# Optimization experiments

Hardware: AMD Instinct MI355X
Metric: run time of the kernel (lower is better)

## Reference

```python
import jax, jax.numpy as jnp
import numpy as np

WS = (7, 7, 7)
NUM_HEADS = 3
DIM = 96
GT_NUM = 1
NW = 64  # number of distinct window masks


def _relative_position_index(ws):
    # Faithful replication of the source's index construction (including its
    # idiosyncratic scale factors 3*ws[1]-1 and 2*ws[1]-1).
    cs = np.arange(ws[0]); ch = np.arange(ws[1]); cw = np.arange(ws[2])
    coords = np.stack(np.meshgrid(cs, ch, cw, indexing='ij'))  # [3, S, H, W]
    cf = coords.reshape(3, -1)                                  # [3, N_]
    rel = cf[:, :, None] - cf[:, None, :]                       # [3, N_, N_]
    rel = rel.transpose(1, 2, 0).copy()
    rel[:, :, 0] += ws[0] - 1
    rel[:, :, 1] += ws[1] - 1
    rel[:, :, 2] += ws[2] - 1
    rel[:, :, 0] *= 3 * ws[1] - 1
    rel[:, :, 1] *= 2 * ws[1] - 1
    return rel.sum(-1).astype(np.int32)                         # [N_, N_]


def setup_inputs() -> dict:
    key = jax.random.key(0)
    ks = jax.random.split(key, 8)
    N_ = WS[0] * WS[1] * WS[2]  # 343
    B_ = 512
    table_size = (2 * WS[0] - 1) * (2 * WS[1] - 1) * (2 * WS[2] - 1)  # 2197
    return {
        'x': jax.random.normal(ks[0], (B_, N_, DIM), jnp.float32),
        'gt': jax.random.normal(ks[1], (B_, GT_NUM, DIM), jnp.float32),
        'mask': jax.random.normal(ks[2], (NW, N_, N_), jnp.float32),
        'rel_index': jnp.asarray(_relative_position_index(WS)),
        'Wqkv': jax.random.normal(ks[3], (3 * DIM, DIM), jnp.float32) * 0.02,
        'b_qkv': jax.random.normal(ks[4], (3 * DIM,), jnp.float32) * 0.02,
        'Wproj': jax.random.normal(ks[5], (DIM, DIM), jnp.float32) * 0.02,
        'b_proj': jax.random.normal(ks[6], (DIM,), jnp.float32) * 0.02,
        'bias_table': jax.random.normal(ks[7], (table_size, NUM_HEADS), jnp.float32) * 0.02,
    }


def reference(x, gt, mask, rel_index, Wqkv, b_qkv, Wproj, b_proj, bias_table):
    B_, N_, C = x.shape
    g = gt.shape[1]
    H = NUM_HEADS
    hd = C // H
    scale = hd ** (-0.5)

    xc = jnp.concatenate([gt, x], axis=1)               # [B_, N, C]
    N = N_ + g
    qkv = xc @ Wqkv.T + b_qkv                           # [B_, N, 3C]
    qkv = qkv.reshape(B_, N, 3, H, hd).transpose(2, 0, 3, 1, 4)
    q, k, v = qkv[0], qkv[1], qkv[2]                    # [B_, H, N, hd]

    attn = jnp.einsum('bhnd,bhmd->bhnm', q * scale, k)  # [B_, H, N, N]

    # gathered relative-position bias: [N_, N_, H] -> [H, N_, N_]
    bias = bias_table[rel_index.reshape(-1)].reshape(N_, N_, H).transpose(2, 0, 1)

    nW = mask.shape[0]
    sub = attn[:, :, g:, g:] + bias[None]               # [B_, H, N_, N_]
    sub = sub.reshape(B_ // nW, nW, H, N_, N_) + mask[None, :, None]
    attn = attn.at[:, :, g:, g:].set(sub.reshape(B_, H, N_, N_))

    attn = jax.nn.softmax(attn, axis=-1)
    out = jnp.einsum('bhnm,bhmd->bhnd', attn, v)        # [B_, H, N, hd]
    out = out.transpose(0, 2, 1, 3).reshape(B_, N, C)
    out = out @ Wproj.T + b_proj

    gt_out = out[:, :-N_, :]
    x_out = out[:, -N_:, :]
    return (x_out, gt_out)
```

## Files before the change

### kernel.cpp

```cpp
#include <hip/hip_runtime.h>

typedef __attribute__((ext_vector_type(8))) _Float16 f16x8;
typedef __fp16 hpk2 __attribute__((ext_vector_type(2)));
typedef __attribute__((ext_vector_type(4))) float f32x4;

#define NB 512
#define NH 3
#define NSEQ 344
#define NPAD 352
#define NX 343
#define HD 32
#define CDIM 96
#define SP 352
#define SP2 (SP * SP)
#define SCALE 0.17677669529663687f

static __device__ __forceinline__ unsigned short f2h(float f) {
    _Float16 h = (_Float16)f;
    return __builtin_bit_cast(unsigned short, h);
}
static __device__ __forceinline__ f16x8 ld8(const unsigned short* p) {
    uint4 u = *(const uint4*)p;
    return __builtin_bit_cast(f16x8, u);
}

__global__ __launch_bounds__(256) void k_bias(
    const int* __restrict__ rel, const float* __restrict__ table,
    const float* __restrict__ mask, float* __restrict__ mp, float* __restrict__ bp)
{
    int idx = blockIdx.x * 256 + threadIdx.x;
    if (idx >= 67 * SP2) return;
    int s = idx / SP2; int rem2 = idx - s * SP2;
    int i = rem2 / SP, jj = rem2 - i * SP;
    bool valid = (i >= 1 && i < NSEQ && jj >= 1 && jj < NSEQ);
    if (s < 64) {
        float v = valid ? mask[(size_t)s * NX * NX + (i - 1) * NX + (jj - 1)] : 0.f;
        mp[(size_t)s * SP2 + rem2] = v;
    } else {
        int h = s - 64;
        float v = 0.f;
        if (valid) { int r = rel[(i - 1) * NX + (jj - 1)]; v = table[r * 3 + h]; }
        bp[(size_t)h * SP2 + rem2] = v;
    }
}

__global__ __launch_bounds__(256) void k_qkv(
    const float* __restrict__ x, const float* __restrict__ gt,
    const float* __restrict__ Wqkv, const float* __restrict__ bqkv,
    unsigned short* __restrict__ qs, unsigned short* __restrict__ ks,
    unsigned short* __restrict__ vs)
{
    __shared__ unsigned short Wb[288 * 104];
    int tid = threadIdx.x;
    for (int i = tid; i < 288 * 96; i += 256) {
        int c = i / 96, k = i - c * 96;
        Wb[c * 104 + k] = f2h(Wqkv[i]);
    }
    __syncthreads();
    int w = tid >> 6, l = tid & 63, la = l & 15, lg = l >> 4;

    int rowA = blockIdx.x * 64 + w * 16 + la;
    int bA = rowA / NSEQ, nA = rowA - bA * NSEQ;
    const float* srcA = (nA == 0) ? (gt + bA * CDIM) : (x + (bA * NX + (nA - 1)) * CDIM);
    f16x8 af[3];
#pragma unroll
    for (int kk = 0; kk < 3; ++kk) {
        float4 f0 = *(const float4*)&srcA[kk * 32 + lg * 8];
        float4 f1 = *(const float4*)&srcA[kk * 32 + lg * 8 + 4];
        f16x8 a;
        a[0] = (_Float16)f0.x; a[1] = (_Float16)f0.y; a[2] = (_Float16)f0.z; a[3] = (_Float16)f0.w;
        a[4] = (_Float16)f1.x; a[5] = (_Float16)f1.y; a[6] = (_Float16)f1.z; a[7] = (_Float16)f1.w;
        af[kk] = a;
    }
    f32x4 acc[18];
#pragma unroll
    for (int t = 0; t < 18; ++t) { acc[t][0]=0.f; acc[t][1]=0.f; acc[t][2]=0.f; acc[t][3]=0.f; }
#pragma unroll
    for (int t = 0; t < 18; ++t) {
#pragma unroll
        for (int kk = 0; kk < 3; ++kk) {
            f16x8 bf = ld8(&Wb[(t * 16 + la) * 104 + kk * 32 + lg * 8]);
            acc[t] = __builtin_amdgcn_mfma_f32_16x16x32_f16(af[kk], bf, acc[t], 0, 0, 0);
        }
    }
    int rowBase = blockIdx.x * 64 + w * 16 + lg * 4;
#pragma unroll
    for (int t = 0; t < 18; ++t) {
        int c = t * 16 + la;
        int s = c / 96;
        int rem = c - s * 96;
        int h = rem >> 5, d = rem & 31;
        float bq = bqkv[c];
        unsigned short* dst = (s == 0) ? qs : ((s == 1) ? ks : vs);
        float mul = (s == 0) ? SCALE : 1.0f;
#pragma unroll
        for (int r = 0; r < 4; ++r) {
            int row = rowBase + r;
            int b = row / NSEQ, n = row - b * NSEQ;
            float v = (acc[t][r] + bq) * mul;
            dst[((b * NH + h) * NPAD + n) * HD + d] = f2h(v);
        }
    }
}

__global__ __launch_bounds__(256) void k_vt(unsigned short* __restrict__ vs)
{
    __shared__ unsigned short Vt[32 * 360];
    int id = blockIdx.x;
    int b = id / NH, h = id - b * NH;
    unsigned short* vb = vs + (size_t)((b * NH + h) * NPAD) * HD;
    int tid = threadIdx.x;
    for (int ch = tid; ch < NSEQ * 4; ch += 256) {
        int n = ch >> 2, dq = ch & 3;
        uint4 raw = *(const uint4*)&vb[n * HD + dq * 8];
        unsigned int uu[4] = {raw.x, raw.y, raw.z, raw.w};
#pragma unroll
        for (int j = 0; j < 4; ++j) {
            Vt[(dq * 8 + 2 * j) * 360 + n]     = (unsigned short)(uu[j] & 0xffffu);
            Vt[(dq * 8 + 2 * j + 1) * 360 + n] = (unsigned short)(uu[j] >> 16);
        }
    }
    __syncthreads();
    for (int ch = tid; ch < 32 * 43; ch += 256) {
        int d = ch / 43, c4 = ch - d * 43;
        uint4 v = *(const uint4*)&Vt[d * 360 + c4 * 8];
        *(uint4*)&vb[d * NSEQ + c4 * 8] = v;
    }
}

template<int NT, int TB, bool PAD>
static __device__ __forceinline__ void attn_chunk(
    const unsigned short* __restrict__ kb, const unsigned short* __restrict__ Vg,
    const float* __restrict__ mrow, const float* __restrict__ brow, int irow,
    f16x8 aq, unsigned short* __restrict__ Pw, int la, int lg,
    float& m_run, float& s_run, f32x4& o0, f32x4& o1)
{
    f32x4 zero4; zero4[0]=0.f; zero4[1]=0.f; zero4[2]=0.f; zero4[3]=0.f;
    f32x4 sc[NT];
#pragma unroll
    for (int t = 0; t < NT; ++t) {
        f16x8 ak = ld8(&kb[((TB + t) * 16 + la) * HD + lg * 8]);
        sc[t] = __builtin_amdgcn_mfma_f32_16x16x32_f16(ak, aq, zero4, 0, 0, 0);
    }
#pragma unroll
    for (int t = 0; t < NT; ++t) {
        int col = (TB + t) * 16 + 4 * lg;
        float4 m4 = *(const float4*)&mrow[irow + col];
        float4 b4 = *(const float4*)&brow[irow + col];
        sc[t][0] += m4.x + b4.x;
        sc[t][1] += m4.y + b4.y;
        sc[t][2] += m4.z + b4.z;
        sc[t][3] += m4.w + b4.w;
    }
    if (PAD) {
#pragma unroll
        for (int r = 0; r < 4; ++r) {
            int j = (TB + NT - 1) * 16 + 4 * lg + r;
            if (j >= NSEQ) sc[NT - 1][r] = -__builtin_inff();
        }
    }
    float cm = fmaxf(fmaxf(sc[0][0], sc[0][1]), fmaxf(sc[0][2], sc[0][3]));
#pragma unroll
    for (int t = 1; t < NT; ++t)
        cm = fmaxf(cm, fmaxf(fmaxf(sc[t][0], sc[t][1]), fmaxf(sc[t][2], sc[t][3])));
    cm = fmaxf(cm, __shfl_xor(cm, 16));
    cm = fmaxf(cm, __shfl_xor(cm, 32));
    float m_new = fmaxf(m_run, cm);
    float scale = __expf(m_run - m_new);
    float cs = 0.f;
#pragma unroll
    for (int t = 0; t < NT; ++t) {
        float p0 = __expf(sc[t][0] - m_new); sc[t][0] = p0;
        float p1 = __expf(sc[t][1] - m_new); sc[t][1] = p1;
        float p2 = __expf(sc[t][2] - m_new); sc[t][2] = p2;
        float p3 = __expf(sc[t][3] - m_new); sc[t][3] = p3;
        cs += (p0 + p1) + (p2 + p3);
    }
    cs += __shfl_xor(cs, 16);
    cs += __shfl_xor(cs, 32);
    s_run = s_run * scale + cs;
    m_run = m_new;
#pragma unroll
    for (int r = 0; r < 4; ++r) {
        float sl = __shfl(scale, 4 * lg + r);
        o0[r] *= sl; o1[r] *= sl;
    }
#pragma unroll
    for (int tt = 0; tt < NT; ++tt) {
        hpk2 plo = __builtin_amdgcn_cvt_pkrtz(sc[tt][0], sc[tt][1]);
        hpk2 phi = __builtin_amdgcn_cvt_pkrtz(sc[tt][2], sc[tt][3]);
        uint2 pk;
        pk.x = __builtin_bit_cast(unsigned int, plo);
        pk.y = __builtin_bit_cast(unsigned int, phi);
        *(uint2*)&Pw[la * 200 + 16 * tt + 4 * lg] = pk;
    }
#pragma unroll
    for (int kk = 0; kk < NT / 2; ++kk) {
        int jn = TB * 16 + kk * 32 + lg * 8;
        f16x8 ap  = ld8(&Pw[la * 200 + kk * 32 + lg * 8]);
        f16x8 bv0 = ld8(&Vg[la * NSEQ + jn]);
        f16x8 bv1 = ld8(&Vg[(16 + la) * NSEQ + jn]);
        o0 = __builtin_amdgcn_mfma_f32_16x16x32_f16(ap, bv0, o0, 0, 0, 0);
        o1 = __builtin_amdgcn_mfma_f32_16x16x32_f16(ap, bv1, o1, 0, 0, 0);
    }
}

__global__ __launch_bounds__(256, 3) void k_attn(
    const unsigned short* __restrict__ qs, const unsigned short* __restrict__ ks,
    const unsigned short* __restrict__ vs, const float* __restrict__ mp,
    const float* __restrict__ bp, unsigned short* __restrict__ ao)
{
    __shared__ unsigned short Pl[4 * 16 * 200];

    int L = blockIdx.x;
    int xcd = L & 7; int s0 = L >> 3;
    int w_loc = s0 / 36; int rem = s0 - w_loc * 36;
    int G = rem / 18; int rem2 = rem - G * 18;
    int h = rem2 / 6; int qt = rem2 - h * 6;
    int wm = xcd + 8 * w_loc;

    int tid = threadIdx.x;
    int w = tid >> 6, l = tid & 63, la = l & 15, lg = l >> 4;
    unsigned short* Pw = Pl + w * 16 * 200;
    const float* mrow = mp + (size_t)wm * SP2;
    const float* brow = bp + (size_t)h * SP2;

    int qrow0 = qt * 64 + w * 16;
    if (qrow0 >= NSEQ) return;

    int irow = (qrow0 + la) * SP;
    int qr = qrow0 + la; if (qr > NX) qr = NX;

    for (int u = 0; u < 4; ++u) {
        int b = wm + 64 * (4 * G + u);
        const unsigned short* qb = qs + (size_t)((b * NH + h) * NPAD) * HD;
        const unsigned short* kb = ks + (size_t)((b * NH + h) * NPAD) * HD;
        const unsigned short* Vg = vs + (size_t)((b * NH + h) * NPAD) * HD;

        f16x8 aq = ld8(&qb[qr * HD + lg * 8]);
        f32x4 o0, o1;
        o0[0]=0.f; o0[1]=0.f; o0[2]=0.f; o0[3]=0.f;
        o1[0]=0.f; o1[1]=0.f; o1[2]=0.f; o1[3]=0.f;
        float m_run = -__builtin_inff(), s_run = 0.f;

        attn_chunk<12, 0, false>(kb, Vg, mrow, brow, irow, aq, Pw, la, lg,
                                 m_run, s_run, o0, o1);
        attn_chunk<10, 12, true>(kb, Vg, mrow, brow, irow, aq, Pw, la, lg,
                                 m_run, s_run, o0, o1);

#pragma unroll
        for (int r = 0; r < 4; ++r) {
            float inv = 1.0f / __shfl(s_run, 4 * lg + r);
            Pw[(lg * 4 + r) * 32 + la]      = f2h(o0[r] * inv);
            Pw[(lg * 4 + r) * 32 + 16 + la] = f2h(o1[r] * inv);
        }
        int row_g = qrow0 + (l >> 2);
        if (row_g < NSEQ) {
            uint4 d = *(const uint4*)&Pw[l * 8];
            unsigned short* dst = ao + ((size_t)(h * NB + b) * NSEQ + row_g) * HD + (l & 3) * 8;
            *(uint4*)dst = d;
        }
    }
}

__global__ __launch_bounds__(256) void k_proj(
    const unsigned short* __restrict__ ao, const float* __restrict__ Wproj,
    const float* __restrict__ bproj, float* __restrict__ out)
{
    __shared__ unsigned short Wb[96 * 104];
    __shared__ float Cs[4][16][100];
    int tid = threadIdx.x;
    for (int i = tid; i < 96 * 96; i += 256) {
        int c = i / 96, k = i - c * 96;
        Wb[c * 104 + k] = f2h(Wproj[i]);
    }
    __syncthreads();
    int w = tid >> 6, l = tid & 63, la = l & 15, lg = l >> 4;
    int rowA = blockIdx.x * 64 + w * 16 + la;
    const size_t HSLAB = (size_t)NB * NSEQ * HD;
    f16x8 af[3];
#pragma unroll
    for (int kk = 0; kk < 3; ++kk)
        af[kk] = ld8(&ao[kk * HSLAB + (size_t)rowA * HD + lg * 8]);
    f32x4 acc[6];
#pragma unroll
    for (int t = 0; t < 6; ++t) { acc[t][0]=0.f; acc[t][1]=0.f; acc[t][2]=0.f; acc[t][3]=0.f; }
#pragma unroll
    for (int t = 0; t < 6; ++t)
#pragma unroll
        for (int kk = 0; kk < 3; ++kk) {
            f16x8 bf = ld8(&Wb[(t * 16 + la) * 104 + kk * 32 + lg * 8]);
            acc[t] = __builtin_amdgcn_mfma_f32_16x16x32_f16(af[kk], bf, acc[t], 0, 0, 0);
        }
#pragma unroll
    for (int t = 0; t < 6; ++t) {
        int c = t * 16 + la;
        float bp_ = bproj[c];
#pragma unroll
        for (int r = 0; r < 4; ++r)
            Cs[w][lg * 4 + r][c] = acc[t][r] + bp_;
    }
    int R0 = blockIdx.x * 64 + w * 16;
    const size_t gt_base = (size_t)NB * NX * CDIM;
#pragma unroll
    for (int k2 = 0; k2 < 6; ++k2) {
        int f4 = k2 * 64 + l;
        int rloc = f4 / 24; int c4 = f4 - rloc * 24;
        int R = R0 + rloc; int bA = R / NSEQ; int nA = R - bA * NSEQ;
        float4 val = *(const float4*)&Cs[w][rloc][c4 * 4];
        float* dst = (nA == 0) ? (out + gt_base + (size_t)bA * CDIM + c4 * 4)
                               : (out + ((size_t)bA * NX + (nA - 1)) * CDIM + c4 * 4);
        *(float4*)dst = val;
    }
}

extern "C" void kernel_launch(void* const* d_in, const int* in_sizes, int n_in,
                              void* d_out, int out_size, void* d_ws, size_t ws_size,
                              hipStream_t stream) {
    const float* x     = (const float*)d_in[0];
    const float* gt    = (const float*)d_in[1];
    const float* mask  = (const float*)d_in[2];
    const int*   rel   = (const int*)d_in[3];
    const float* Wqkv  = (const float*)d_in[4];
    const float* bqkv  = (const float*)d_in[5];
    const float* Wproj = (const float*)d_in[6];
    const float* bproj = (const float*)d_in[7];
    const float* table = (const float*)d_in[8];
    float* out = (float*)d_out;

    size_t qkv_elems = (size_t)NB * NH * NPAD * HD;
    unsigned short* qs = (unsigned short*)d_ws;
    unsigned short* ks = qs + qkv_elems;
    unsigned short* vs = ks + qkv_elems;
    unsigned short* ao = vs + qkv_elems;
    float* mp = (float*)(ao + (size_t)NH * NB * NSEQ * HD);
    float* bp = mp + (size_t)64 * SP2;

    hipLaunchKernelGGL(k_bias, dim3((67 * SP2 + 255) / 256), dim3(256), 0, stream,
                       rel, table, mask, mp, bp);
    hipLaunchKernelGGL(k_qkv, dim3(2752), dim3(256), 0, stream,
                       x, gt, Wqkv, bqkv, qs, ks, vs);
    hipLaunchKernelGGL(k_vt, dim3(NB * NH), dim3(256), 0, stream, vs);
    hipLaunchKernelGGL(k_attn, dim3(2304), dim3(256), 0, stream,
                       qs, ks, vs, mp, bp, ao);
    hipLaunchKernelGGL(k_proj, dim3(2752), dim3(256), 0, stream,
                       ao, Wproj, bproj, out);
    (void)in_sizes; (void)n_in; (void)out_size; (void)ws_size;
}
```

Baseline: 413.2 us.

## Fuse V transpose into QKV kernel and switch softmax to exp2 domain

Removes the separate k_vt kernel. The QKV projection now stages V rows in shared memory and writes them out transposed directly. Q scale, mask and bias are pre-multiplied by log2(e) so the softmax can use exp2f instead of __expf. This saves one kernel launch plus a full read/write pass over V, and a multiply per exponential. In exchange k_qkv needs about 72 KB of dynamic shared memory, which may reduce occupancy, and the transposed V stores are 2-byte scattered writes.

```diff
diff --git a/kernel.cpp b/kernel.cpp
--- a/kernel.cpp
+++ b/kernel.cpp
@@ -14,6 +14,7 @@
 #define SP 352
 #define SP2 (SP * SP)
 #define SCALE 0.17677669529663687f
+#define LOG2E 1.4426950408889634f
 
 static __device__ __forceinline__ unsigned short f2h(float f) {
     _Float16 h = (_Float16)f;
@@ -34,12 +35,12 @@
     int i = rem2 / SP, jj = rem2 - i * SP;
     bool valid = (i >= 1 && i < NSEQ && jj >= 1 && jj < NSEQ);
     if (s < 64) {
-        float v = valid ? mask[(size_t)s * NX * NX + (i - 1) * NX + (jj - 1)] : 0.f;
+        float v = valid ? LOG2E * mask[(size_t)s * NX * NX + (i - 1) * NX + (jj - 1)] : 0.f;
         mp[(size_t)s * SP2 + rem2] = v;
     } else {
         int h = s - 64;
         float v = 0.f;
-        if (valid) { int r = rel[(i - 1) * NX + (jj - 1)]; v = table[r * 3 + h]; }
+        if (valid) { int r = rel[(i - 1) * NX + (jj - 1)]; v = LOG2E * table[r * 3 + h]; }
         bp[(size_t)h * SP2 + rem2] = v;
     }
 }
@@ -50,7 +51,9 @@
     unsigned short* __restrict__ qs, unsigned short* __restrict__ ks,
     unsigned short* __restrict__ vs)
 {
-    __shared__ unsigned short Wb[288 * 104];
+    extern __shared__ char smem[];
+    unsigned short* Wb  = (unsigned short*)smem;
+    unsigned short* Vst = (unsigned short*)(smem + 59904);
     int tid = threadIdx.x;
     for (int i = tid; i < 288 * 96; i += 256) {
         int c = i / 96, k = i - c * 96;
@@ -91,40 +94,26 @@
         int rem = c - s * 96;
         int h = rem >> 5, d = rem & 31;
         float bq = bqkv[c];
-        unsigned short* dst = (s == 0) ? qs : ((s == 1) ? ks : vs);
-        float mul = (s == 0) ? SCALE : 1.0f;
 #pragma unroll
         for (int r = 0; r < 4; ++r) {
-            int row = rowBase + r;
-            int b = row / NSEQ, n = row - b * NSEQ;
-            float v = (acc[t][r] + bq) * mul;
-            dst[((b * NH + h) * NPAD + n) * HD + d] = f2h(v);
-        }
-    }
-}
-
-__global__ __launch_bounds__(256) void k_vt(unsigned short* __restrict__ vs)
-{
-    __shared__ unsigned short Vt[32 * 360];
-    int id = blockIdx.x;
-    int b = id / NH, h = id - b * NH;
-    unsigned short* vb = vs + (size_t)((b * NH + h) * NPAD) * HD;
-    int tid = threadIdx.x;
-    for (int ch = tid; ch < NSEQ * 4; ch += 256) {
-        int n = ch >> 2, dq = ch & 3;
-        uint4 raw = *(const uint4*)&vb[n * HD + dq * 8];
-        unsigned int uu[4] = {raw.x, raw.y, raw.z, raw.w};
-#pragma unroll
-        for (int j = 0; j < 4; ++j) {
-            Vt[(dq * 8 + 2 * j) * 360 + n]     = (unsigned short)(uu[j] & 0xffffu);
-            Vt[(dq * 8 + 2 * j + 1) * 360 + n] = (unsigned short)(uu[j] >> 16);
+            if (s == 2) {
+                Vst[(w * 16 + lg * 4 + r) * 100 + rem] = f2h(acc[t][r] + bq);
+            } else {
+                int row = rowBase + r;
+                int b = row / NSEQ, n = row - b * NSEQ;
+                float mul = (s == 0) ? (SCALE * LOG2E) : 1.0f;
+                unsigned short* dst = (s == 0) ? qs : ks;
+                dst[((b * NH + h) * NPAD + n) * HD + d] = f2h((acc[t][r] + bq) * mul);
+            }
         }
     }
     __syncthreads();
-    for (int ch = tid; ch < 32 * 43; ch += 256) {
-        int d = ch / 43, c4 = ch - d * 43;
-        uint4 v = *(const uint4*)&Vt[d * 360 + c4 * 8];
-        *(uint4*)&vb[d * NSEQ + c4 * 8] = v;
+    for (int it = 0; it < 24; ++it) {
+        int c2 = it * 4 + w;
+        int hh = c2 >> 5, dd = c2 & 31;
+        int row = blockIdx.x * 64 + l;
+        int bb = row / NSEQ, nn = row - bb * NSEQ;
+        vs[(size_t)((bb * NH + hh) * NPAD) * HD + dd * NSEQ + nn] = Vst[l * 100 + c2];
     }
 }
 
@@ -166,14 +155,14 @@
     cm = fmaxf(cm, __shfl_xor(cm, 16));
     cm = fmaxf(cm, __shfl_xor(cm, 32));
     float m_new = fmaxf(m_run, cm);
-    float scale = __expf(m_run - m_new);
+    float scale = exp2f(m_run - m_new);
     float cs = 0.f;
 #pragma unroll
     for (int t = 0; t < NT; ++t) {
-        float p0 = __expf(sc[t][0] - m_new); sc[t][0] = p0;
-        float p1 = __expf(sc[t][1] - m_new); sc[t][1] = p1;
-        float p2 = __expf(sc[t][2] - m_new); sc[t][2] = p2;
-        float p3 = __expf(sc[t][3] - m_new); sc[t][3] = p3;
+        float p0 = exp2f(sc[t][0] - m_new); sc[t][0] = p0;
+        float p1 = exp2f(sc[t][1] - m_new); sc[t][1] = p1;
+        float p2 = exp2f(sc[t][2] - m_new); sc[t][2] = p2;
+        float p3 = exp2f(sc[t][3] - m_new); sc[t][3] = p3;
         cs += (p0 + p1) + (p2 + p3);
     }
     cs += __shfl_xor(cs, 16);
@@ -338,9 +327,8 @@
 
     hipLaunchKernelGGL(k_bias, dim3((67 * SP2 + 255) / 256), dim3(256), 0, stream,
                        rel, table, mask, mp, bp);
-    hipLaunchKernelGGL(k_qkv, dim3(2752), dim3(256), 0, stream,
+    hipLaunchKernelGGL(k_qkv, dim3(2752), dim3(256), 72704, stream,
                        x, gt, Wqkv, bqkv, qs, ks, vs);
-    hipLaunchKernelGGL(k_vt, dim3(NB * NH), dim3(256), 0, stream, vs);
     hipLaunchKernelGGL(k_attn, dim3(2304), dim3(256), 0, stream,
                        qs, ks, vs, mp, bp, ao);
     hipLaunchKernelGGL(k_proj, dim3(2752), dim3(256), 0, stream,
```

Measured after the change: 459.1 us. +11.1%, slower.
